# Kernel tuning notes

Measured on AMD Instinct MI355X. Metric: run time of the kernel, lower is better.

The kernel has to match this reference:

```python
import jax, jax.numpy as jnp
import numpy as np

B, S, HID = 2, 2048, 2048
NH, NKV, D = 16, 8, 128
N_REP = NH // NKV
EPS = 1e-6
THETA = 10000.0


def setup_inputs() -> dict:
    key = jax.random.key(0)
    ks = jax.random.split(key, 6)
    s = 0.02
    return {
        "hidden_states": jax.random.normal(ks[0], (B, S, HID), jnp.float32),
        "attention_mask": jnp.ones((B, S), jnp.float32),
        "wq": jax.random.normal(ks[1], (HID, NH * D), jnp.float32) * s,
        "wk": jax.random.normal(ks[2], (HID, NKV * D), jnp.float32) * s,
        "wv": jax.random.normal(ks[3], (HID, NKV * D), jnp.float32) * s,
        "wo": jax.random.normal(ks[4], (NH * D, HID), jnp.float32) * s,
        "q_norm_w": jnp.ones((D,), jnp.float32),
        "k_norm_w": jnp.ones((D,), jnp.float32),
    }


def _rms_norm(x, w, eps=EPS):
    # x: (..., D); computed in fp32 like the torch module
    x32 = x.astype(jnp.float32)
    var = jnp.mean(x32 * x32, axis=-1, keepdims=True)
    return (w * (x32 * jax.lax.rsqrt(var + eps))).astype(x.dtype)


def _rotate_half(x):
    x1, x2 = jnp.split(x, 2, axis=-1)
    return jnp.concatenate((-x2, x1), axis=-1)


def _rope_cos_sin(seq_len, dim, dtype):
    inv_freq = 1.0 / (THETA ** (jnp.arange(0, dim, 2, dtype=jnp.float32) / dim))
    t = jnp.arange(seq_len, dtype=jnp.float32)
    freqs = t[:, None] * inv_freq[None, :]          # (S, D/2)
    emb = jnp.concatenate((freqs, freqs), axis=-1)  # (S, D)
    # broadcast to (1, 1, S, D)
    return jnp.cos(emb).astype(dtype)[None, None], jnp.sin(emb).astype(dtype)[None, None]


def reference(hidden_states, attention_mask, wq, wk, wv, wo, q_norm_w, k_norm_w):
    b, s, _ = hidden_states.shape
    # QKV projections (bias-free)
    q = (hidden_states @ wq).reshape(b, s, NH, D).transpose(0, 2, 1, 3)   # (b, nh, s, d)
    k = (hidden_states @ wk).reshape(b, s, NKV, D).transpose(0, 2, 1, 3)  # (b, nkv, s, d)
    v = (hidden_states @ wv).reshape(b, s, NKV, D).transpose(0, 2, 1, 3)
    # per-head QK RMSNorm
    q = _rms_norm(q, q_norm_w)
    k = _rms_norm(k, k_norm_w)
    # RoPE
    cos, sin = _rope_cos_sin(s, D, q.dtype)
    q = q * cos + _rotate_half(q) * sin
    k = k * cos + _rotate_half(k) * sin
    # GQA repeat kv heads
    k = jnp.repeat(k, N_REP, axis=1)
    v = jnp.repeat(v, N_REP, axis=1)
    # SDPA (bidirectional, additive padding mask)
    scale = 1.0 / np.sqrt(D)
    scores = jnp.einsum("bhqd,bhkd->bhqk", q, k) * scale
    add_mask = (1.0 - attention_mask)[:, None, None, :] * jnp.finfo(scores.dtype).min
    scores = scores + add_mask
    attn = jax.nn.softmax(scores, axis=-1)
    out = jnp.einsum("bhqk,bhkd->bhqd", attn, v)
    out = out.transpose(0, 2, 1, 3).reshape(b, s, NH * D)
    return out @ wo
```

## Files before the change

### kernel.cpp

```cpp
#include <hip/hip_runtime.h>
#include <stdint.h>

#define BB   2
#define SS   2048
#define HID  2048
#define NHQ  16
#define NKV  8
#define DD   128
#define QKVW 4096

typedef __bf16 v8bf   __attribute__((ext_vector_type(8)));
typedef float  f32x4  __attribute__((ext_vector_type(4)));
typedef float  f32x16 __attribute__((ext_vector_type(16)));

__device__ __forceinline__ float bf2f(ushort u) {
    union { unsigned int i; float f; } x; x.i = ((unsigned int)u) << 16; return x.f;
}
__device__ __forceinline__ ushort f2bf(float f) {
    union { float f; unsigned int i; } x; x.f = f;
    unsigned int i = x.i;
    return (ushort)((i + 0x7fffu + ((i >> 16) & 1u)) >> 16);
}
__device__ __forceinline__ v8bf as_bf8(uint4 u) { return __builtin_bit_cast(v8bf, u); }

__device__ __forceinline__ unsigned int cvtpk_bf16(float lo, float hi) {
    unsigned int r;
    asm("v_cvt_pk_bf16_f32 %0, %1, %2" : "=v"(r) : "v"(lo), "v"(hi));
    return r;
}

__device__ __forceinline__ void store_el(float* p, float v)  { *p = v; }
__device__ __forceinline__ void store_el(ushort* p, float v) { *p = f2bf(v); }

__device__ __forceinline__ void gll16(const ushort* g, ushort* l) {
    __builtin_amdgcn_global_load_lds(
        (const __attribute__((address_space(1))) void*)g,
        (__attribute__((address_space(3))) void*)l, 16, 0, 0);
}

__device__ __forceinline__ int swz_off(int r, int lcolb) {
    return r * 64 + (((lcolb) ^ ((r & 4) << 3)) >> 1);
}

#define PREP_CAST   8192
#define PREP_WQ     (PREP_CAST)
#define PREP_WK     (PREP_WQ + 4096)
#define PREP_WV     (PREP_WK + 2048)
#define PREP_WO     (PREP_WV + 2048)
#define PREP_TOTAL  (PREP_WO + 4096)

__device__ __forceinline__ void tcast_body(
    const float* __restrict__ in, ushort* __restrict__ out,
    int K, int N, int bx, int by, int t)
{
    __shared__ float tile[32][33];
    int n0 = bx * 32, k0 = by * 32;
    int tx = t & 31, ty = t >> 5;
#pragma unroll
    for (int i = 0; i < 32; i += 8)
        tile[ty + i][tx] = in[(size_t)(k0 + ty + i) * N + n0 + tx];
    __syncthreads();
#pragma unroll
    for (int i = 0; i < 32; i += 8)
        out[(size_t)(n0 + ty + i) * K + k0 + tx] = f2bf(tile[tx][ty + i]);
}

__global__ __launch_bounds__(256) void prep(
    const float* __restrict__ X,  const float* __restrict__ wq,
    const float* __restrict__ wk, const float* __restrict__ wv,
    const float* __restrict__ wo,
    ushort* __restrict__ Xb, ushort* __restrict__ WqkvT, ushort* __restrict__ Wot)
{
    int bid = blockIdx.x, t = threadIdx.x;
    if (bid < PREP_CAST) {
        int i = (bid * 256 + t) * 4;
        float4 v = *(const float4*)&X[i];
        ushort4 o = { f2bf(v.x), f2bf(v.y), f2bf(v.z), f2bf(v.w) };
        *(ushort4*)&Xb[i] = o;
    } else if (bid < PREP_WK) {
        int l = bid - PREP_WQ;
        tcast_body(wq, WqkvT, 2048, 2048, l & 63, l >> 6, t);
    } else if (bid < PREP_WV) {
        int l = bid - PREP_WK;
        tcast_body(wk, WqkvT + (size_t)2048 * 2048, 2048, 1024, l & 31, l >> 5, t);
    } else if (bid < PREP_WO) {
        int l = bid - PREP_WV;
        tcast_body(wv, WqkvT + (size_t)3072 * 2048, 2048, 1024, l & 31, l >> 5, t);
    } else {
        int l = bid - PREP_WO;
        tcast_body(wo, Wot, 2048, 2048, l & 63, l >> 6, t);
    }
}

template <typename OutT>
__global__ __launch_bounds__(512, 2) void gemm_bt2(
    const ushort* __restrict__ A, const ushort* __restrict__ Bt,
    OutT* __restrict__ C, int M, int N, int K)
{
    __shared__ __align__(16) ushort As[3][256 * 64];
    __shared__ __align__(16) ushort Bs[3][128 * 64];
    const int t = threadIdx.x;
    const int lane = t & 63, wave = t >> 6;
    const int quad = lane >> 4, l15 = lane & 15;
    const int m0 = blockIdx.y * 256, n0 = blockIdx.x * 128;
    const int wm = (wave >> 1) * 64;
    const int wn = (wave & 1) * 64;

    const f32x4 zv = {0.f, 0.f, 0.f, 0.f};
    f32x4 acc[4][4];
#pragma unroll
    for (int i = 0; i < 4; i++)
#pragma unroll
        for (int j = 0; j < 4; j++) acc[i][j] = zv;

    int arow[4], acol[4];
#pragma unroll
    for (int j = 0; j < 4; j++) {
        int p = (j * 512 + t) * 16;
        int l = p ^ (((p >> 9) & 1) << 5);
        arow[j] = l >> 7; acol[j] = (l & 127) >> 1;
    }
    int brow[2], bcol[2];
#pragma unroll
    for (int j = 0; j < 2; j++) {
        int p = (j * 512 + t) * 16;
        int l = p ^ (((p >> 9) & 1) << 5);
        brow[j] = l >> 7; bcol[j] = (l & 127) >> 1;
    }

    int aoff[4][2], boff[2][2][2];
#pragma unroll
    for (int mf = 0; mf < 4; mf++)
#pragma unroll
        for (int kk = 0; kk < 2; kk++)
            aoff[mf][kk] = swz_off(wm + mf * 16 + l15, kk * 64 + quad * 16);
#pragma unroll
    for (int q = 0; q < 2; q++)
#pragma unroll
        for (int nf = 0; nf < 2; nf++)
#pragma unroll
            for (int kk = 0; kk < 2; kk++)
                boff[q][nf][kk] = swz_off(wn + q * 32 + nf * 16 + l15, kk * 64 + quad * 16);

#define STAGE_A(j, slot, kk0) \
    gll16(&A[(size_t)(m0 + arow[j]) * K + (kk0) + acol[j]], &As[slot][0] + ((j) * 512 + t) * 8)
#define STAGE_B(j, slot, kk0) \
    gll16(&Bt[(size_t)(n0 + brow[j]) * K + (kk0) + bcol[j]], &Bs[slot][0] + ((j) * 512 + t) * 8)

    const int NT = K >> 6;

#pragma unroll
    for (int j = 0; j < 4; j++) STAGE_A(j, 0, 0);
#pragma unroll
    for (int j = 0; j < 2; j++) STAGE_B(j, 0, 0);
#pragma unroll
    for (int j = 0; j < 4; j++) STAGE_A(j, 1, 64);
#pragma unroll
    for (int j = 0; j < 2; j++) STAGE_B(j, 1, 64);
    asm volatile("s_waitcnt vmcnt(6)" ::: "memory");
    __builtin_amdgcn_s_barrier();

    int cur = 0;
    for (int T = 0; T < NT; T++) {
        const ushort* Ac = &As[cur][0];
        const ushort* Bc = &Bs[cur][0];
        int stg = cur + 2; if (stg >= 3) stg -= 3;
        const int k2 = (T + 2) << 6;
        const bool do_stage = (T + 2) < NT;

        uint4 af[4][2], bf[2][2];
#pragma unroll
        for (int mf = 0; mf < 4; mf++)
#pragma unroll
            for (int kk = 0; kk < 2; kk++)
                af[mf][kk] = *(const uint4*)&Ac[aoff[mf][kk]];
#pragma unroll
        for (int nf = 0; nf < 2; nf++)
#pragma unroll
            for (int kk = 0; kk < 2; kk++)
                bf[nf][kk] = *(const uint4*)&Bc[boff[0][nf][kk]];
        if (do_stage) {
            STAGE_A(0, stg, k2); STAGE_A(1, stg, k2); STAGE_B(0, stg, k2);
        }
        __builtin_amdgcn_s_barrier();
        asm volatile("s_waitcnt lgkmcnt(0)" ::: "memory");
        __builtin_amdgcn_sched_barrier(0);
        __builtin_amdgcn_s_setprio(1);
#pragma unroll
        for (int mf = 0; mf < 4; mf++)
#pragma unroll
            for (int nf = 0; nf < 2; nf++)
#pragma unroll
                for (int kk = 0; kk < 2; kk++)
                    acc[mf][nf] = __builtin_amdgcn_mfma_f32_16x16x32_bf16(
                        as_bf8(af[mf][kk]), as_bf8(bf[nf][kk]), acc[mf][nf], 0, 0, 0);
        __builtin_amdgcn_s_setprio(0);
        __builtin_amdgcn_s_barrier();

#pragma unroll
        for (int nf = 0; nf < 2; nf++)
#pragma unroll
            for (int kk = 0; kk < 2; kk++)
                bf[nf][kk] = *(const uint4*)&Bc[boff[1][nf][kk]];
        if (do_stage) {
            STAGE_A(2, stg, k2); STAGE_A(3, stg, k2); STAGE_B(1, stg, k2);
            asm volatile("s_waitcnt vmcnt(6)" ::: "memory");
        } else if (T + 2 == NT) {
            asm volatile("s_waitcnt vmcnt(0)" ::: "memory");
        }
        __builtin_amdgcn_s_barrier();
        asm volatile("s_waitcnt lgkmcnt(0)" ::: "memory");
        __builtin_amdgcn_sched_barrier(0);
        __builtin_amdgcn_s_setprio(1);
#pragma unroll
        for (int mf = 0; mf < 4; mf++)
#pragma unroll
            for (int nf = 0; nf < 2; nf++)
#pragma unroll
                for (int kk = 0; kk < 2; kk++)
                    acc[mf][2 + nf] = __builtin_amdgcn_mfma_f32_16x16x32_bf16(
                        as_bf8(af[mf][kk]), as_bf8(bf[nf][kk]), acc[mf][2 + nf], 0, 0, 0);
        __builtin_amdgcn_s_setprio(0);
        __builtin_amdgcn_s_barrier();

        cur++; if (cur == 3) cur = 0;
    }
#undef STAGE_A
#undef STAGE_B

#pragma unroll
    for (int mf = 0; mf < 4; mf++)
#pragma unroll
        for (int nf = 0; nf < 4; nf++)
#pragma unroll
            for (int r = 0; r < 4; r++) {
                int row = m0 + wm + mf * 16 + quad * 4 + r;
                int col = n0 + wn + nf * 16 + l15;
                store_el(&C[(size_t)row * N + col], acc[mf][nf][r]);
            }
}

__global__ __launch_bounds__(256) void norm_rope(
    ushort* __restrict__ qkv, const float* __restrict__ qw, const float* __restrict__ kw)
{
    int row = blockIdx.x;
    int s = row & (SS - 1);
    int lane = threadIdx.x & 63, wave = threadIdx.x >> 6;
    int l = lane & 31, hsel = lane >> 5;
    float d0 = (float)(2 * l), d1 = d0 + 1.0f;
    float inv0 = expf(-d0 * (1.0f / 64.0f) * 9.210340371976184f);
    float inv1 = expf(-d1 * (1.0f / 64.0f) * 9.210340371976184f);
    float c0, s0, c1, s1;
    sincosf((float)s * inv0, &s0, &c0);
    sincosf((float)s * inv1, &s1, &c1);
    float qw0 = qw[2 * l], qw1 = qw[2 * l + 1], qy0 = qw[2 * l + 64], qy1 = qw[2 * l + 65];
    float kw0 = kw[2 * l], kw1 = kw[2 * l + 1], ky0 = kw[2 * l + 64], ky1 = kw[2 * l + 65];

#pragma unroll
    for (int pass = 0; pass < 3; pass++) {
        int h = pass * 8 + wave * 2 + hsel;
        ushort* p = qkv + (size_t)row * QKVW + h * 128;
        unsigned int ulo = *(const unsigned int*)&p[2 * l];
        unsigned int uhi = *(const unsigned int*)&p[2 * l + 64];
        float x0 = bf2f((ushort)ulo), x1 = bf2f((ushort)(ulo >> 16));
        float y0 = bf2f((ushort)uhi), y1 = bf2f((ushort)(uhi >> 16));
        float ssum = x0 * x0 + x1 * x1 + y0 * y0 + y1 * y1;
#pragma unroll
        for (int xm = 1; xm < 32; xm <<= 1) ssum += __shfl_xor(ssum, xm, 64);
        float r = rsqrtf(ssum * (1.0f / 128.0f) + 1e-6f);
        bool isq = (h < 16);
        float w0 = isq ? qw0 : kw0, w1 = isq ? qw1 : kw1;
        float v0 = isq ? qy0 : ky0, v1 = isq ? qy1 : ky1;
        float sc = isq ? 0.08838834764831845f : 1.0f;
        float nx0 = w0 * (x0 * r), nx1 = w1 * (x1 * r);
        float ny0 = v0 * (y0 * r), ny1 = v1 * (y1 * r);
        float ox0 = (nx0 * c0 - ny0 * s0) * sc, ox1 = (nx1 * c1 - ny1 * s1) * sc;
        float oy0 = (ny0 * c0 + nx0 * s0) * sc, oy1 = (ny1 * c1 + nx1 * s1) * sc;
        *(unsigned int*)&p[2 * l]      = (unsigned int)f2bf(ox0) | ((unsigned int)f2bf(ox1) << 16);
        *(unsigned int*)&p[2 * l + 64] = (unsigned int)f2bf(oy0) | ((unsigned int)f2bf(oy1) << 16);
    }
}

__global__ __launch_bounds__(256, 2) void flash_attn(
    const ushort* __restrict__ qkv, const float* __restrict__ mask, ushort* __restrict__ O)
{
    __shared__ __align__(16) ushort Ks[64 * 128];
    __shared__ __align__(16) ushort Vt[128 * 64];
    __shared__ __align__(16) float  Madd[SS];
    const int t = threadIdx.x;
    const int lane = t & 63, wave = t >> 6;
    const int l31 = lane & 31, half = lane >> 5;
    const int b = blockIdx.z, h = blockIdx.y, q0 = blockIdx.x * 128;
    const int kh = h >> 1;

#pragma unroll
    for (int i = 0; i < 2; i++) {
        int idx = i * 1024 + t * 4;
        float4 mv = *(const float4*)&mask[b * SS + idx];
        float4 o = { (1.f - mv.x) * -1e30f, (1.f - mv.y) * -1e30f,
                     (1.f - mv.z) * -1e30f, (1.f - mv.w) * -1e30f };
        *(float4*)&Madd[idx] = o;
    }

    uint4 aq[8];
    {
        const ushort* qp = qkv + ((size_t)(b * SS + q0 + wave * 32 + l31)) * QKVW + h * 128 + half * 8;
#pragma unroll
        for (int kt = 0; kt < 8; kt++) aq[kt] = *(const uint4*)&qp[kt * 16];
    }
    f32x16 acc_o[4];
#pragma unroll
    for (int i = 0; i < 4; i++)
#pragma unroll
        for (int r = 0; r < 16; r++) acc_o[i][r] = 0.f;
    float lp[4] = {0.f, 0.f, 0.f, 0.f};

    const ushort* Kg = qkv + (size_t)b * SS * QKVW + 2048 + kh * 128;
    const ushort* Vg = qkv + (size_t)b * SS * QKVW + 3072 + kh * 128;

    const int vp = t & 31, vdc = t >> 5;
    uint4 vreg[4];
#define LOAD_V(K0)                                                                  \
    {                                                                               \
        _Pragma("unroll")                                                           \
        for (int pass = 0; pass < 2; pass++) {                                      \
            int d0 = (vdc + pass * 8) * 8;                                          \
            vreg[pass * 2 + 0] = *(const uint4*)&Vg[(size_t)((K0) + 2 * vp) * QKVW + d0];     \
            vreg[pass * 2 + 1] = *(const uint4*)&Vg[(size_t)((K0) + 2 * vp + 1) * QKVW + d0]; \
        }                                                                           \
    }
    LOAD_V(0);

    for (int k0 = 0; k0 < SS; k0 += 64) {
        __syncthreads();
#pragma unroll
        for (int i = 0; i < 4; i++) {
            int chunk = i * 256 + t;
            int row = chunk >> 4, cp = chunk & 15;
            int cl = cp ^ (row & 15);
            gll16(&Kg[(size_t)(k0 + row) * QKVW + cl * 8], &Ks[chunk * 8]);
        }
#pragma unroll
        for (int pass = 0; pass < 2; pass++) {
            const ushort* pa_ = (const ushort*)&vreg[pass * 2 + 0];
            const ushort* pb_ = (const ushort*)&vreg[pass * 2 + 1];
            int d0 = (vdc + pass * 8) * 8;
#pragma unroll
            for (int j = 0; j < 8; j++) {
                int cp = (vp >> 2) ^ j;
                unsigned int v = (unsigned int)pa_[j] | ((unsigned int)pb_[j] << 16);
                *(unsigned int*)&Vt[(d0 + j) * 64 + cp * 8 + (vp & 3) * 2] = v;
            }
        }
        __syncthreads();
        if (k0 + 64 < SS) LOAD_V(k0 + 64);

        f32x16 sc[2];
        __builtin_amdgcn_s_setprio(1);
#pragma unroll
        for (int nt = 0; nt < 2; nt++) {
#pragma unroll
            for (int r = 0; r < 16; r++) sc[nt][r] = 0.f;
#pragma unroll
            for (int kt = 0; kt < 8; kt++) {
                int cp = (kt * 2 + half) ^ (l31 & 15);
                uint4 bk = *(const uint4*)&Ks[(nt * 32 + l31) * 128 + cp * 8];
                sc[nt] = __builtin_amdgcn_mfma_f32_32x32x16_bf16(
                    as_bf8(bk), as_bf8(aq[kt]), sc[nt], 0, 0, 0);
            }
        }
        __builtin_amdgcn_s_setprio(0);

        uint4 pa[4];
#pragma unroll
        for (int nt = 0; nt < 2; nt++) {
            float p[16];
#pragma unroll
            for (int g = 0; g < 4; g++) {
                f32x4 em = *(const f32x4*)&Madd[k0 + nt * 32 + 4 * half + g * 8];
#pragma unroll
                for (int j = 0; j < 4; j++) {
                    int r = g * 4 + j;
                    float pv = __expf(sc[nt][r] + em[j]);
                    p[r] = pv;
                    lp[j] += pv;
                }
            }
            unsigned int pk[8];
#pragma unroll
            for (int i = 0; i < 8; i++) pk[i] = cvtpk_bf16(p[2 * i], p[2 * i + 1]);
            auto sA = __builtin_amdgcn_permlane32_swap(pk[0], pk[2], false, false);
            auto sB = __builtin_amdgcn_permlane32_swap(pk[1], pk[3], false, false);
            auto sC = __builtin_amdgcn_permlane32_swap(pk[4], pk[6], false, false);
            auto sD = __builtin_amdgcn_permlane32_swap(pk[5], pk[7], false, false);
            uint4 f0, f1;
            f0.x = sA[0]; f0.y = sB[0]; f0.z = sA[1]; f0.w = sB[1];
            f1.x = sC[0]; f1.y = sD[0]; f1.z = sC[1]; f1.w = sD[1];
            pa[nt * 2 + 0] = f0;
            pa[nt * 2 + 1] = f1;
        }

        __builtin_amdgcn_s_setprio(1);
#pragma unroll
        for (int kt2 = 0; kt2 < 4; kt2++) {
            int kc = kt2 * 2 + half;
            int co = (kc ^ (l31 & 7)) * 8;
#pragma unroll
            for (int nt = 0; nt < 4; nt++) {
                uint4 bv = *(const uint4*)&Vt[(nt * 32 + l31) * 64 + co];
                acc_o[nt] = __builtin_amdgcn_mfma_f32_32x32x16_bf16(
                    as_bf8(pa[kt2]), as_bf8(bv), acc_o[nt], 0, 0, 0);
            }
        }
        __builtin_amdgcn_s_setprio(0);
    }
    float lsum = (lp[0] + lp[1]) + (lp[2] + lp[3]);
    lsum += __shfl_xor(lsum, 32, 64);
    float linv = 1.0f / lsum;
    float li[16];
#pragma unroll
    for (int r = 0; r < 16; r++)
        li[r] = __shfl(linv, (r & 3) + 8 * (r >> 2) + 4 * half, 64);
#pragma unroll
    for (int nt = 0; nt < 4; nt++)
#pragma unroll
        for (int r = 0; r < 16; r++) {
            int prow = (r & 3) + 8 * (r >> 2) + 4 * half;
            int qrow = q0 + wave * 32 + prow;
            int d = nt * 32 + l31;
            float v = acc_o[nt][r] * li[r];
            O[((size_t)(b * SS + qrow)) * (NHQ * DD) + h * 128 + d] = f2bf(v);
        }
}

extern "C" void kernel_launch(void* const* d_in, const int* in_sizes, int n_in,
                              void* d_out, int out_size, void* d_ws, size_t ws_size,
                              hipStream_t stream)
{
    const float* X    = (const float*)d_in[0];
    const float* mask = (const float*)d_in[1];
    const float* wq   = (const float*)d_in[2];
    const float* wk   = (const float*)d_in[3];
    const float* wv   = (const float*)d_in[4];
    const float* wo   = (const float*)d_in[5];
    const float* qnw  = (const float*)d_in[6];
    const float* knw  = (const float*)d_in[7];
    float* out = (float*)d_out;

    const size_t M = (size_t)BB * SS;
    ushort* Xb    = (ushort*)d_ws;
    ushort* WqkvT = Xb    + M * HID;
    ushort* Wot   = WqkvT + (size_t)4096 * HID;
    ushort* QKV   = Wot   + (size_t)2048 * 2048;
    ushort* Obuf  = QKV   + M * QKVW;

    prep<<<PREP_TOTAL, 256, 0, stream>>>(X, wq, wk, wv, wo, Xb, WqkvT, Wot);

    gemm_bt2<ushort><<<dim3(4096 / 128, 4096 / 256), 512, 0, stream>>>(Xb, WqkvT, QKV, 4096, 4096, 2048);

    norm_rope<<<(int)M, 256, 0, stream>>>(QKV, qnw, knw);

    flash_attn<<<dim3(SS / 128, NHQ, BB), 256, 0, stream>>>(QKV, mask, Obuf);

    gemm_bt2<float><<<dim3(2048 / 128, 4096 / 256), 512, 0, stream>>>(Obuf, Wot, out, 4096, 2048, 2048);
}
```

Measured before the change: 352.3 us.

## Double-buffer K tiles in LDS and fold log2e scale and mask into scores

K tiles are now staged into a two-slot LDS buffer, so the next tile's async global-to-LDS load is issued one iteration ahead and overlaps the current QK^T and PV work. The second full __syncthreads is replaced by an LDS-only waitcnt plus a raw s_barrier. The Q scale now also carries log2(e), so softmax can use the hardware exp2. The additive mask is loaded as the initial score accumulator, which removes an add per element. The cost is an extra 16 KB of LDS, which may limit occupancy, and the correctness of the barrier now depends on the top-of-loop __syncthreads draining the prefetched K loads.

After: 345.0 us. -2.1%, faster.

```diff
diff --git a/kernel.cpp b/kernel.cpp
--- a/kernel.cpp
+++ b/kernel.cpp
@@ -271,7 +271,7 @@
         bool isq = (h < 16);
         float w0 = isq ? qw0 : kw0, w1 = isq ? qw1 : kw1;
         float v0 = isq ? qy0 : ky0, v1 = isq ? qy1 : ky1;
-        float sc = isq ? 0.08838834764831845f : 1.0f;
+        float sc = isq ? (0.08838834764831845f * 1.4426950408889634f) : 1.0f;
         float nx0 = w0 * (x0 * r), nx1 = w1 * (x1 * r);
         float ny0 = v0 * (y0 * r), ny1 = v1 * (y1 * r);
         float ox0 = (nx0 * c0 - ny0 * s0) * sc, ox1 = (nx1 * c1 - ny1 * s1) * sc;
@@ -284,7 +284,7 @@
 __global__ __launch_bounds__(256, 2) void flash_attn(
     const ushort* __restrict__ qkv, const float* __restrict__ mask, ushort* __restrict__ O)
 {
-    __shared__ __align__(16) ushort Ks[64 * 128];
+    __shared__ __align__(16) ushort Ks[2][64 * 128];
     __shared__ __align__(16) ushort Vt[128 * 64];
     __shared__ __align__(16) float  Madd[SS];
     const int t = threadIdx.x;
@@ -329,17 +329,24 @@
             vreg[pass * 2 + 1] = *(const uint4*)&Vg[(size_t)((K0) + 2 * vp + 1) * QKVW + d0]; \
         }                                                                           \
     }
+#define STAGE_K(K0, buf)                                                            \
+    {                                                                               \
+        _Pragma("unroll")                                                           \
+        for (int i = 0; i < 4; i++) {                                               \
+            int chunk = i * 256 + t;                                                \
+            int row = chunk >> 4, cp = chunk & 15;                                  \
+            int cl = cp ^ (row & 15);                                               \
+            gll16(&Kg[(size_t)((K0) + row) * QKVW + cl * 8], &Ks[buf][chunk * 8]);  \
+        }                                                                           \
+    }
+
+    STAGE_K(0, 0);
     LOAD_V(0);
 
     for (int k0 = 0; k0 < SS; k0 += 64) {
+        const int cur = (k0 >> 6) & 1;
         __syncthreads();
-#pragma unroll
-        for (int i = 0; i < 4; i++) {
-            int chunk = i * 256 + t;
-            int row = chunk >> 4, cp = chunk & 15;
-            int cl = cp ^ (row & 15);
-            gll16(&Kg[(size_t)(k0 + row) * QKVW + cl * 8], &Ks[chunk * 8]);
-        }
+        if (k0 + 64 < SS) STAGE_K(k0 + 64, cur ^ 1);
 #pragma unroll
         for (int pass = 0; pass < 2; pass++) {
             const ushort* pa_ = (const ushort*)&vreg[pass * 2 + 0];
@@ -352,19 +359,27 @@
                 *(unsigned int*)&Vt[(d0 + j) * 64 + cp * 8 + (vp & 3) * 2] = v;
             }
         }
-        __syncthreads();
         if (k0 + 64 < SS) LOAD_V(k0 + 64);
+        asm volatile("s_waitcnt lgkmcnt(0)" ::: "memory");
+        __builtin_amdgcn_sched_barrier(0);
+        __builtin_amdgcn_s_barrier();
 
         f32x16 sc[2];
+#pragma unroll
+        for (int nt = 0; nt < 2; nt++)
+#pragma unroll
+            for (int g = 0; g < 4; g++) {
+                f32x4 em = *(const f32x4*)&Madd[k0 + nt * 32 + 4 * half + g * 8];
+#pragma unroll
+                for (int j = 0; j < 4; j++) sc[nt][g * 4 + j] = em[j];
+            }
         __builtin_amdgcn_s_setprio(1);
 #pragma unroll
         for (int nt = 0; nt < 2; nt++) {
-#pragma unroll
-            for (int r = 0; r < 16; r++) sc[nt][r] = 0.f;
 #pragma unroll
             for (int kt = 0; kt < 8; kt++) {
                 int cp = (kt * 2 + half) ^ (l31 & 15);
-                uint4 bk = *(const uint4*)&Ks[(nt * 32 + l31) * 128 + cp * 8];
+                uint4 bk = *(const uint4*)&Ks[cur][(nt * 32 + l31) * 128 + cp * 8];
                 sc[nt] = __builtin_amdgcn_mfma_f32_32x32x16_bf16(
                     as_bf8(bk), as_bf8(aq[kt]), sc[nt], 0, 0, 0);
             }
@@ -376,15 +391,10 @@
         for (int nt = 0; nt < 2; nt++) {
             float p[16];
 #pragma unroll
-            for (int g = 0; g < 4; g++) {
-                f32x4 em = *(const f32x4*)&Madd[k0 + nt * 32 + 4 * half + g * 8];
-#pragma unroll
-                for (int j = 0; j < 4; j++) {
-                    int r = g * 4 + j;
-                    float pv = __expf(sc[nt][r] + em[j]);
-                    p[r] = pv;
-                    lp[j] += pv;
-                }
+            for (int r = 0; r < 16; r++) {
+                float pv = __builtin_amdgcn_exp2f(sc[nt][r]);
+                p[r] = pv;
+                lp[r & 3] += pv;
             }
             unsigned int pk[8];
 #pragma unroll
```
